# Optimization experiments

Measured on AMD Instinct MI355X. Metric: run time of the kernel, lower is better.

The kernel has to match this reference:

```python
import jax, jax.numpy as jnp
import numpy as np

N_NODES = 100000
N_EDGES = 3200000
IN_C, HID_C, OUT_C = 64, 64, 32


def setup_inputs() -> dict:
    key = jax.random.key(0)
    ks = jax.random.split(key, 8)
    x = jax.random.normal(ks[0], (N_NODES, IN_C), dtype=jnp.float32)
    edge_index = jax.random.randint(ks[1], (2, N_EDGES), 0, N_NODES, dtype=jnp.int64)
    s1 = 1.0 / np.sqrt(IN_C)
    s2 = 1.0 / np.sqrt(HID_C)
    W1l = jax.random.uniform(ks[2], (IN_C, HID_C), jnp.float32, -s1, s1)
    b1l = jnp.zeros((HID_C,), jnp.float32)
    W1r = jax.random.uniform(ks[3], (IN_C, HID_C), jnp.float32, -s1, s1)
    W2l = jax.random.uniform(ks[4], (HID_C, OUT_C), jnp.float32, -s2, s2)
    b2l = jnp.zeros((OUT_C,), jnp.float32)
    W2r = jax.random.uniform(ks[5], (HID_C, OUT_C), jnp.float32, -s2, s2)
    return {"x": x, "edge_index": edge_index, "W1l": W1l, "b1l": b1l,
            "W1r": W1r, "W2l": W2l, "b2l": b2l, "W2r": W2r}


def _sage_conv(x, src, dst, Wl, bl, Wr):
    # mean-aggregate source features onto destination nodes
    msg = x[src]                                              # [E, d] gather
    summed = jax.ops.segment_sum(msg, dst, num_segments=N_NODES)
    deg = jax.ops.segment_sum(jnp.ones((src.shape[0],), x.dtype), dst,
                              num_segments=N_NODES)
    agg = summed / jnp.maximum(deg, 1.0)[:, None]             # [N, d]
    return agg @ Wl + bl + x @ Wr                             # lin_l(agg)+lin_r(x)


def reference(x, edge_index, W1l, b1l, W1r, W2l, b2l, W2r):
    src, dst = edge_index[0], edge_index[1]
    h = jax.nn.relu(_sage_conv(x, src, dst, W1l, b1l, W1r))
    # dropout is identity in eval mode
    return _sage_conv(h, src, dst, W2l, b2l, W2r)
```

## Files before the change

### kernel.cpp

```cpp
#include <hip/hip_runtime.h>
#include <hip/hip_bf16.h>

#define N_NODES 100000
#define N_EDGES 3200000
#define NBKT 391
#define BKT_CAP 10240

typedef __hip_bfloat16 bf16;
typedef unsigned int uint;
typedef __attribute__((ext_vector_type(8))) short bf16x8;
typedef __attribute__((ext_vector_type(4))) float f32x4;

__device__ __forceinline__ float b2f(bf16 v) { return __bfloat162float(v); }

__device__ __forceinline__ float bits2f(unsigned short w) {
    union { unsigned short u; bf16 b; } c;
    c.u = w;
    return __bfloat162float(c.b);
}
__device__ __forceinline__ unsigned short f2bits(float f) {
    return (unsigned short)(__float_as_uint(f) >> 16);
}
__device__ __forceinline__ unsigned short f2bf_bits(float f) {
    bf16 b = __float2bfloat16(f);
    unsigned short u;
    __builtin_memcpy(&u, &b, 2);
    return u;
}

__device__ __forceinline__ int get_idx(const void* ei, long long pos, int is64) {
    if (is64) return (int)((const long long*)ei)[pos];
    return ((const int*)ei)[pos];
}
__device__ __forceinline__ float get_f(const void* p, long long pos, int isbf) {
    if (isbf) return b2f(((const bf16*)p)[pos]);
    return ((const float*)p)[pos];
}

__global__ void detect_kernel(const void* __restrict__ x,
                              const void* __restrict__ ei,
                              int* __restrict__ flags) {
    int lane = threadIdx.x;
    const unsigned short* xw = (const unsigned short*)x;
    float v = bits2f(xw[2 * lane]);
    bool plaus = (v == v) && fabsf(v) > 1e-3f && fabsf(v) < 1e2f;
    unsigned long long m1 = __ballot(plaus);
    const int* iw = (const int*)ei;
    bool z = (iw[2 * lane + 1] == 0);
    unsigned long long m2 = __ballot(z);
    if (lane == 0) {
        flags[0] = (__popcll(m1) >= 32) ? 1 : 0;
        flags[1] = (__popcll(m2) == 64) ? 1 : 0;
    }
}

__global__ __launch_bounds__(256) void scatterA_kernel(
    const void* __restrict__ ei, int* __restrict__ bucket_cursor,
    uint* __restrict__ bucket_data, const int* __restrict__ flags) {
    __shared__ int lhist[NBKT];
    __shared__ int lbase[NBKT];
    int is64 = flags[1];
    int t = threadIdx.x;
    int chunk0 = blockIdx.x * 8192;

    for (int i = t; i < NBKT; i += 256) lhist[i] = 0;
    __syncthreads();
    for (int j = 0; j < 32; j++) {
        int e = chunk0 + j * 256 + t;
        if (e < N_EDGES) {
            int d = get_idx(ei, (long long)N_EDGES + e, is64);
            atomicAdd(&lhist[d >> 8], 1);
        }
    }
    __syncthreads();
    for (int i = t; i < NBKT; i += 256) {
        int c = lhist[i];
        lbase[i] = c ? atomicAdd(&bucket_cursor[i], c) : 0;
        lhist[i] = 0;
    }
    __syncthreads();
    for (int j = 0; j < 32; j++) {
        int e = chunk0 + j * 256 + t;
        if (e < N_EDGES) {
            int s = get_idx(ei, e, is64);
            int d = get_idx(ei, (long long)N_EDGES + e, is64);
            int b = d >> 8;
            int o = lbase[b] + atomicAdd(&lhist[b], 1);
            if (o < BKT_CAP)
                bucket_data[(long long)b * BKT_CAP + o] = ((uint)(d & 255) << 17) | (uint)s;
        }
    }
}

__global__ void scanBuckets_kernel(const int* __restrict__ cnt,
                                   int* __restrict__ base) {
    __shared__ int buf[512];
    int t = threadIdx.x;
    int v = (t < NBKT) ? cnt[t] : 0;
    buf[t] = v;
    __syncthreads();
    for (int off = 1; off < 512; off <<= 1) {
        int add = (t >= off) ? buf[t - off] : 0;
        __syncthreads();
        buf[t] += add;
        __syncthreads();
    }
    if (t < NBKT) base[t] = buf[t] - v;
}

__global__ __launch_bounds__(256) void csrB_kernel(
    const int* __restrict__ bucket_cnt, const int* __restrict__ bucket_base,
    const uint* __restrict__ bucket_data, int* __restrict__ csr_src,
    int* __restrict__ row_start) {
    __shared__ int lh[256];
    __shared__ int buf[256];
    int b = blockIdx.x;
    int t = threadIdx.x;
    int cnt = bucket_cnt[b];
    if (cnt > BKT_CAP) cnt = BKT_CAP;
    int base = bucket_base[b];
    const uint* bd = bucket_data + (long long)b * BKT_CAP;

    lh[t] = 0;
    __syncthreads();
    for (int i = t; i < cnt; i += 256) atomicAdd(&lh[bd[i] >> 17], 1);
    __syncthreads();
    int v = lh[t];
    buf[t] = v;
    __syncthreads();
    for (int off = 1; off < 256; off <<= 1) {
        int add = (t >= off) ? buf[t - off] : 0;
        __syncthreads();
        buf[t] += add;
        __syncthreads();
    }
    int excl = buf[t] - v;
    int g = (b << 8) + t;
    if (g < N_NODES) row_start[g] = base + excl;
    lh[t] = excl;
    __syncthreads();
    for (int i = t; i < cnt; i += 256) {
        uint e = bd[i];
        int o = atomicAdd(&lh[e >> 17], 1);
        csr_src[base + o] = (int)(e & 0x1FFFFu);
    }
    if (b == 0 && t == 0) row_start[N_NODES] = N_EDGES;
}

__global__ __launch_bounds__(256) void node1_kernel(
    const void* __restrict__ x, const int* __restrict__ row_start,
    const int* __restrict__ csr_src, const void* __restrict__ W1l,
    const void* __restrict__ b1l, const void* __restrict__ W1r,
    const void* __restrict__ W2l, const void* __restrict__ b2l,
    const void* __restrict__ W2r, bf16* __restrict__ zbuf,
    bf16* __restrict__ rbuf, const int* __restrict__ flags) {
    __shared__ __align__(16) unsigned short sW1t[64][136];
    __shared__ __align__(16) unsigned short sA[64][136];
    __shared__ __align__(16) unsigned short sW2t[64][72];
    __shared__ __align__(16) unsigned short sH[64][72];
    __shared__ float sB1[64];
    __shared__ float sB2[32];

    int isbf = flags[0];
    int t = threadIdx.x;

    for (int i = t; i < 64 * 128; i += 256) {
        int n = i & 63, k = i >> 6;
        unsigned short v;
        if (isbf)
            v = (k < 64) ? ((const unsigned short*)W1l)[k * 64 + n]
                         : ((const unsigned short*)W1r)[(k - 64) * 64 + n];
        else
            v = f2bits((k < 64) ? ((const float*)W1l)[k * 64 + n]
                                : ((const float*)W1r)[(k - 64) * 64 + n]);
        sW1t[n][k] = v;
    }
    for (int i = t; i < 64 * 64; i += 256) {
        int n = i & 63, k = i >> 6;
        unsigned short v;
        if (isbf)
            v = (n < 32) ? ((const unsigned short*)W2l)[k * 32 + n]
                         : ((const unsigned short*)W2r)[k * 32 + (n - 32)];
        else
            v = f2bits((n < 32) ? ((const float*)W2l)[k * 32 + n]
                                : ((const float*)W2r)[k * 32 + (n - 32)]);
        sW2t[n][k] = v;
    }
    if (t < 64) sB1[t] = get_f(b1l, t, isbf);
    if (t < 32) sB2[t] = get_f(b2l, t, isbf);

    int w = t >> 6, lane = t & 63;
    int mbase = w * 16;
    int n0 = blockIdx.x * 64;
    const uint4* xr4 = (const uint4*)x;
    int e8 = lane >> 3, q8 = lane & 7;
    int e4 = lane >> 4, q16 = lane & 15;

    for (int i = 0; i < 16; i++) {
        int m = mbase + i;
        int n = n0 + m;
        float acc[8] = {0, 0, 0, 0, 0, 0, 0, 0};
        int dg = 0;
        int start = 0, end = 0;
        if (n < N_NODES) {
            start = row_start[n];
            end = row_start[n + 1];
            dg = end - start;
        }
        float av = 0.0f, xv = 0.0f;
        if (isbf) {
            for (int base = start; base < end; base += 32) {
                int i0 = base + e8, i1 = i0 + 8, i2 = i0 + 16, i3 = i0 + 24;
                int s0 = (i0 < end) ? csr_src[i0] : -1;
                int s1 = (i1 < end) ? csr_src[i1] : -1;
                int s2 = (i2 < end) ? csr_src[i2] : -1;
                int s3 = (i3 < end) ? csr_src[i3] : -1;
                uint4 v0 = {0,0,0,0}, v1 = {0,0,0,0}, v2 = {0,0,0,0}, v3 = {0,0,0,0};
                if (s0 >= 0) v0 = xr4[s0 * 8 + q8];
                if (s1 >= 0) v1 = xr4[s1 * 8 + q8];
                if (s2 >= 0) v2 = xr4[s2 * 8 + q8];
                if (s3 >= 0) v3 = xr4[s3 * 8 + q8];
                acc[0] += __uint_as_float(v0.x << 16) + __uint_as_float(v1.x << 16)
                        + __uint_as_float(v2.x << 16) + __uint_as_float(v3.x << 16);
                acc[1] += __uint_as_float(v0.x & 0xffff0000u) + __uint_as_float(v1.x & 0xffff0000u)
                        + __uint_as_float(v2.x & 0xffff0000u) + __uint_as_float(v3.x & 0xffff0000u);
                acc[2] += __uint_as_float(v0.y << 16) + __uint_as_float(v1.y << 16)
                        + __uint_as_float(v2.y << 16) + __uint_as_float(v3.y << 16);
                acc[3] += __uint_as_float(v0.y & 0xffff0000u) + __uint_as_float(v1.y & 0xffff0000u)
                        + __uint_as_float(v2.y & 0xffff0000u) + __uint_as_float(v3.y & 0xffff0000u);
                acc[4] += __uint_as_float(v0.z << 16) + __uint_as_float(v1.z << 16)
                        + __uint_as_float(v2.z << 16) + __uint_as_float(v3.z << 16);
                acc[5] += __uint_as_float(v0.z & 0xffff0000u) + __uint_as_float(v1.z & 0xffff0000u)
                        + __uint_as_float(v2.z & 0xffff0000u) + __uint_as_float(v3.z & 0xffff0000u);
                acc[6] += __uint_as_float(v0.w << 16) + __uint_as_float(v1.w << 16)
                        + __uint_as_float(v2.w << 16) + __uint_as_float(v3.w << 16);
                acc[7] += __uint_as_float(v0.w & 0xffff0000u) + __uint_as_float(v1.w & 0xffff0000u)
                        + __uint_as_float(v2.w & 0xffff0000u) + __uint_as_float(v3.w & 0xffff0000u);
            }
#pragma unroll
            for (int mm = 8; mm <= 32; mm <<= 1)
#pragma unroll
                for (int k = 0; k < 8; k++) acc[k] += __shfl_xor(acc[k], mm, 64);
#pragma unroll
            for (int k = 0; k < 8; k++) {
                float v = __shfl(acc[k], lane >> 3, 64);
                av = ((lane & 7) == k) ? v : av;
            }
            if (n < N_NODES) xv = b2f(((const bf16*)x)[(long long)n * 64 + lane]);
        } else {
            const uint4* xf = (const uint4*)x;
            for (int base = start; base < end; base += 16) {
                int i0 = base + e4, i1 = i0 + 4, i2 = i0 + 8, i3 = i0 + 12;
                int s0 = (i0 < end) ? csr_src[i0] : -1;
                int s1 = (i1 < end) ? csr_src[i1] : -1;
                int s2 = (i2 < end) ? csr_src[i2] : -1;
                int s3 = (i3 < end) ? csr_src[i3] : -1;
                uint4 v0 = {0,0,0,0}, v1 = {0,0,0,0}, v2 = {0,0,0,0}, v3 = {0,0,0,0};
                if (s0 >= 0) v0 = xf[s0 * 16 + q16];
                if (s1 >= 0) v1 = xf[s1 * 16 + q16];
                if (s2 >= 0) v2 = xf[s2 * 16 + q16];
                if (s3 >= 0) v3 = xf[s3 * 16 + q16];
                acc[0] += __uint_as_float(v0.x) + __uint_as_float(v1.x)
                        + __uint_as_float(v2.x) + __uint_as_float(v3.x);
                acc[1] += __uint_as_float(v0.y) + __uint_as_float(v1.y)
                        + __uint_as_float(v2.y) + __uint_as_float(v3.y);
                acc[2] += __uint_as_float(v0.z) + __uint_as_float(v1.z)
                        + __uint_as_float(v2.z) + __uint_as_float(v3.z);
                acc[3] += __uint_as_float(v0.w) + __uint_as_float(v1.w)
                        + __uint_as_float(v2.w) + __uint_as_float(v3.w);
            }
#pragma unroll
            for (int mm = 16; mm <= 32; mm <<= 1)
#pragma unroll
                for (int k = 0; k < 4; k++) acc[k] += __shfl_xor(acc[k], mm, 64);
#pragma unroll
            for (int k = 0; k < 4; k++) {
                float v = __shfl(acc[k], lane >> 2, 64);
                av = ((lane & 3) == k) ? v : av;
            }
            if (n < N_NODES) xv = ((const float*)x)[(long long)n * 64 + lane];
        }
        av *= 1.0f / fmaxf((float)dg, 1.0f);
        sA[m][lane] = f2bf_bits(av);
        sA[m][64 + lane] = f2bf_bits(xv);
    }
    __syncthreads();

    int q = lane >> 4, r15 = lane & 15;
    f32x4 acc1[4] = {{0,0,0,0},{0,0,0,0},{0,0,0,0},{0,0,0,0}};
#pragma unroll
    for (int ks = 0; ks < 4; ks++) {
        bf16x8 afrag = *(const bf16x8*)&sA[mbase + r15][ks * 32 + q * 8];
#pragma unroll
        for (int nt = 0; nt < 4; nt++) {
            bf16x8 bfrag = *(const bf16x8*)&sW1t[nt * 16 + r15][ks * 32 + q * 8];
            acc1[nt] = __builtin_amdgcn_mfma_f32_16x16x32_bf16(afrag, bfrag, acc1[nt], 0, 0, 0);
        }
    }
#pragma unroll
    for (int nt = 0; nt < 4; nt++) {
        int col = nt * 16 + r15;
        float bias = sB1[col];
#pragma unroll
        for (int rr = 0; rr < 4; rr++) {
            int m = mbase + q * 4 + rr;
            sH[m][col] = f2bf_bits(fmaxf(acc1[nt][rr] + bias, 0.0f));
        }
    }
    __syncthreads();

    f32x4 acc2[4] = {{0,0,0,0},{0,0,0,0},{0,0,0,0},{0,0,0,0}};
#pragma unroll
    for (int ks = 0; ks < 2; ks++) {
        bf16x8 afrag = *(const bf16x8*)&sH[mbase + r15][ks * 32 + q * 8];
#pragma unroll
        for (int nt = 0; nt < 4; nt++) {
            bf16x8 bfrag = *(const bf16x8*)&sW2t[nt * 16 + r15][ks * 32 + q * 8];
            acc2[nt] = __builtin_amdgcn_mfma_f32_16x16x32_bf16(afrag, bfrag, acc2[nt], 0, 0, 0);
        }
    }
#pragma unroll
    for (int nt = 0; nt < 4; nt++) {
        int col = nt * 16 + r15;
#pragma unroll
        for (int rr = 0; rr < 4; rr++) {
            int m = mbase + q * 4 + rr;
            int n = n0 + m;
            if (n < N_NODES) {
                float v = acc2[nt][rr];
                if (col < 32)
                    zbuf[(long long)n * 32 + col] = __float2bfloat16(v);
                else
                    rbuf[(long long)n * 32 + (col - 32)] = __float2bfloat16(v + sB2[col - 32]);
            }
        }
    }
}

__global__ void node2_kernel(const int* __restrict__ row_start,
                             const int* __restrict__ csr_src,
                             const bf16* __restrict__ z,
                             const bf16* __restrict__ rbuf,
                             void* __restrict__ out,
                             const int* __restrict__ flags) {
    int isbf = flags[0];
    int t = threadIdx.x;
    int lane = t & 63;
    int e = lane >> 2, q = lane & 3;
    int gw = (blockIdx.x * blockDim.x + t) >> 6;
    int nwaves = (gridDim.x * blockDim.x) >> 6;
    const uint4* zr = (const uint4*)z;

    for (int n = gw; n < N_NODES; n += nwaves) {
        int start = row_start[n];
        int end = row_start[n + 1];
        float acc[8] = {0, 0, 0, 0, 0, 0, 0, 0};
        for (int base = start; base < end; base += 32) {
            int i0 = base + e, i1 = base + 16 + e;
            int s0 = (i0 < end) ? csr_src[i0] : -1;
            int s1 = (i1 < end) ? csr_src[i1] : -1;
            uint4 v0 = {0, 0, 0, 0}, v1 = {0, 0, 0, 0};
            if (s0 >= 0) v0 = zr[s0 * 4 + q];
            if (s1 >= 0) v1 = zr[s1 * 4 + q];
            acc[0] += __uint_as_float(v0.x << 16) + __uint_as_float(v1.x << 16);
            acc[1] += __uint_as_float(v0.x & 0xffff0000u) + __uint_as_float(v1.x & 0xffff0000u);
            acc[2] += __uint_as_float(v0.y << 16) + __uint_as_float(v1.y << 16);
            acc[3] += __uint_as_float(v0.y & 0xffff0000u) + __uint_as_float(v1.y & 0xffff0000u);
            acc[4] += __uint_as_float(v0.z << 16) + __uint_as_float(v1.z << 16);
            acc[5] += __uint_as_float(v0.z & 0xffff0000u) + __uint_as_float(v1.z & 0xffff0000u);
            acc[6] += __uint_as_float(v0.w << 16) + __uint_as_float(v1.w << 16);
            acc[7] += __uint_as_float(v0.w & 0xffff0000u) + __uint_as_float(v1.w & 0xffff0000u);
        }
#pragma unroll
        for (int m = 4; m <= 32; m <<= 1)
#pragma unroll
            for (int k = 0; k < 8; k++) acc[k] += __shfl_xor(acc[k], m, 64);
        float sv = 0.0f;
#pragma unroll
        for (int k = 0; k < 8; k++) {
            float v = __shfl(acc[k], lane >> 3, 64);
            sv = ((lane & 7) == k) ? v : sv;
        }
        if (lane < 32) {
            float invd = 1.0f / fmaxf((float)(end - start), 1.0f);
            float val = sv * invd + b2f(rbuf[n * 32 + lane]);
            if (isbf)
                ((bf16*)out)[n * 32 + lane] = __float2bfloat16(val);
            else
                ((float*)out)[n * 32 + lane] = val;
        }
    }
}

extern "C" void kernel_launch(void* const* d_in, const int* in_sizes, int n_in,
                              void* d_out, int out_size, void* d_ws, size_t ws_size,
                              hipStream_t stream) {
    const void* x = d_in[0];
    const void* ei = d_in[1];
    const void* W1l = d_in[2];
    const void* b1l = d_in[3];
    const void* W1r = d_in[4];
    const void* W2l = d_in[5];
    const void* b2l = d_in[6];
    const void* W2r = d_in[7];

    char* ws = (char*)d_ws;
    uint* bucket_data = (uint*)ws;
    int* csr_src = (int*)(ws + 16015424);
    int* row_start = (int*)(ws + 28815424);
    int* bucket_cursor = (int*)(ws + 29215488);
    int* bucket_base = (int*)(ws + 29217088);
    bf16* zbuf = (bf16*)(ws + 29218688);
    bf16* rbuf = (bf16*)(ws + 35618688);
    int* flags = (int*)(ws + 42018688);

    hipMemsetAsync(bucket_cursor, 0, NBKT * 4, stream);

    detect_kernel<<<1, 64, 0, stream>>>(x, ei, flags);
    scatterA_kernel<<<NBKT, 256, 0, stream>>>(ei, bucket_cursor, bucket_data, flags);
    scanBuckets_kernel<<<1, 512, 0, stream>>>(bucket_cursor, bucket_base);
    csrB_kernel<<<NBKT, 256, 0, stream>>>(bucket_cursor, bucket_base, bucket_data,
                                          csr_src, row_start);
    node1_kernel<<<1563, 256, 0, stream>>>(x, row_start, csr_src, W1l, b1l, W1r,
                                           W2l, b2l, W2r, zbuf, rbuf, flags);
    node2_kernel<<<8192, 256, 0, stream>>>(row_start, csr_src, zbuf, rbuf, d_out,
                                           flags);
}
```

Before: 411.4 us.

## Split layer-1 gather from GEMM into separate kernels with wave-per-node grid

After: 377.0 us. -8.4%, faster.

```diff
diff --git a/kernel.cpp b/kernel.cpp
--- a/kernel.cpp
+++ b/kernel.cpp
@@ -147,67 +147,25 @@
     if (b == 0 && t == 0) row_start[N_NODES] = N_EDGES;
 }
 
-__global__ __launch_bounds__(256) void node1_kernel(
+__global__ __launch_bounds__(256) void gather1_kernel(
     const void* __restrict__ x, const int* __restrict__ row_start,
-    const int* __restrict__ csr_src, const void* __restrict__ W1l,
-    const void* __restrict__ b1l, const void* __restrict__ W1r,
-    const void* __restrict__ W2l, const void* __restrict__ b2l,
-    const void* __restrict__ W2r, bf16* __restrict__ zbuf,
-    bf16* __restrict__ rbuf, const int* __restrict__ flags) {
-    __shared__ __align__(16) unsigned short sW1t[64][136];
-    __shared__ __align__(16) unsigned short sA[64][136];
-    __shared__ __align__(16) unsigned short sW2t[64][72];
-    __shared__ __align__(16) unsigned short sH[64][72];
-    __shared__ float sB1[64];
-    __shared__ float sB2[32];
-
+    const int* __restrict__ csr_src, bf16* __restrict__ aggbuf,
+    const int* __restrict__ flags) {
     int isbf = flags[0];
     int t = threadIdx.x;
-
-    for (int i = t; i < 64 * 128; i += 256) {
-        int n = i & 63, k = i >> 6;
-        unsigned short v;
-        if (isbf)
-            v = (k < 64) ? ((const unsigned short*)W1l)[k * 64 + n]
-                         : ((const unsigned short*)W1r)[(k - 64) * 64 + n];
-        else
-            v = f2bits((k < 64) ? ((const float*)W1l)[k * 64 + n]
-                                : ((const float*)W1r)[(k - 64) * 64 + n]);
-        sW1t[n][k] = v;
-    }
-    for (int i = t; i < 64 * 64; i += 256) {
-        int n = i & 63, k = i >> 6;
-        unsigned short v;
-        if (isbf)
-            v = (n < 32) ? ((const unsigned short*)W2l)[k * 32 + n]
-                         : ((const unsigned short*)W2r)[k * 32 + (n - 32)];
-        else
-            v = f2bits((n < 32) ? ((const float*)W2l)[k * 32 + n]
-                                : ((const float*)W2r)[k * 32 + (n - 32)]);
-        sW2t[n][k] = v;
-    }
-    if (t < 64) sB1[t] = get_f(b1l, t, isbf);
-    if (t < 32) sB2[t] = get_f(b2l, t, isbf);
-
-    int w = t >> 6, lane = t & 63;
-    int mbase = w * 16;
-    int n0 = blockIdx.x * 64;
-    const uint4* xr4 = (const uint4*)x;
+    int lane = t & 63;
+    int gw = (blockIdx.x * 256 + t) >> 6;
+    int nw = (gridDim.x * 256) >> 6;
     int e8 = lane >> 3, q8 = lane & 7;
     int e4 = lane >> 4, q16 = lane & 15;
-
-    for (int i = 0; i < 16; i++) {
-        int m = mbase + i;
-        int n = n0 + m;
+    const uint4* xr4 = (const uint4*)x;
+
+    for (int n = gw; n < N_NODES; n += nw) {
+        int start = row_start[n];
+        int end = row_start[n + 1];
+        int dg = end - start;
         float acc[8] = {0, 0, 0, 0, 0, 0, 0, 0};
-        int dg = 0;
-        int start = 0, end = 0;
-        if (n < N_NODES) {
-            start = row_start[n];
-            end = row_start[n + 1];
-            dg = end - start;
-        }
-        float av = 0.0f, xv = 0.0f;
+        float av = 0.0f;
         if (isbf) {
             for (int base = start; base < end; base += 32) {
                 int i0 = base + e8, i1 = i0 + 8, i2 = i0 + 16, i3 = i0 + 24;
@@ -246,7 +204,6 @@
                 float v = __shfl(acc[k], lane >> 3, 64);
                 av = ((lane & 7) == k) ? v : av;
             }
-            if (n < N_NODES) xv = b2f(((const bf16*)x)[(long long)n * 64 + lane]);
         } else {
             const uint4* xf = (const uint4*)x;
             for (int base = start; base < end; base += 16) {
@@ -278,14 +235,82 @@
                 float v = __shfl(acc[k], lane >> 2, 64);
                 av = ((lane & 3) == k) ? v : av;
             }
-            if (n < N_NODES) xv = ((const float*)x)[(long long)n * 64 + lane];
         }
         av *= 1.0f / fmaxf((float)dg, 1.0f);
-        sA[m][lane] = f2bf_bits(av);
-        sA[m][64 + lane] = f2bf_bits(xv);
-    }
-    __syncthreads();
-
+        aggbuf[(long long)n * 64 + lane] = __float2bfloat16(av);
+    }
+}
+
+__global__ __launch_bounds__(256) void gemm1_kernel(
+    const void* __restrict__ x, const bf16* __restrict__ aggbuf,
+    const void* __restrict__ W1l, const void* __restrict__ b1l,
+    const void* __restrict__ W1r, const void* __restrict__ W2l,
+    const void* __restrict__ b2l, const void* __restrict__ W2r,
+    bf16* __restrict__ zbuf, bf16* __restrict__ rbuf,
+    const int* __restrict__ flags) {
+    __shared__ __align__(16) unsigned short sW1t[64][136];
+    __shared__ __align__(16) unsigned short sA[64][136];
+    __shared__ __align__(16) unsigned short sW2t[64][72];
+    __shared__ __align__(16) unsigned short sH[64][72];
+    __shared__ float sB1[64];
+    __shared__ float sB2[32];
+
+    int isbf = flags[0];
+    int t = threadIdx.x;
+    int n0 = blockIdx.x * 64;
+
+    for (int i = t; i < 64 * 128; i += 256) {
+        int n = i & 63, k = i >> 6;
+        unsigned short v;
+        if (isbf)
+            v = (k < 64) ? ((const unsigned short*)W1l)[k * 64 + n]
+                         : ((const unsigned short*)W1r)[(k - 64) * 64 + n];
+        else
+            v = f2bits((k < 64) ? ((const float*)W1l)[k * 64 + n]
+                                : ((const float*)W1r)[(k - 64) * 64 + n]);
+        sW1t[n][k] = v;
+    }
+    for (int i = t; i < 64 * 64; i += 256) {
+        int n = i & 63, k = i >> 6;
+        unsigned short v;
+        if (isbf)
+            v = (n < 32) ? ((const unsigned short*)W2l)[k * 32 + n]
+                         : ((const unsigned short*)W2r)[k * 32 + (n - 32)];
+        else
+            v = f2bits((n < 32) ? ((const float*)W2l)[k * 32 + n]
+                                : ((const float*)W2r)[k * 32 + (n - 32)]);
+        sW2t[n][k] = v;
+    }
+    if (t < 64) sB1[t] = get_f(b1l, t, isbf);
+    if (t < 32) sB2[t] = get_f(b2l, t, isbf);
+
+    const uint4* ag4 = (const uint4*)aggbuf;
+    if (isbf) {
+        const uint4* x4 = (const uint4*)x;
+        for (int i = t; i < 64 * 16; i += 256) {
+            int m = i >> 4, c = i & 15;
+            int nn = min(n0 + m, N_NODES - 1);
+            uint4 v = (c < 8) ? ag4[(long long)nn * 8 + c]
+                              : x4[(long long)nn * 8 + (c - 8)];
+            *(uint4*)&sA[m][c * 8] = v;
+        }
+    } else {
+        for (int i = t; i < 64 * 8; i += 256) {
+            int m = i >> 3, c = i & 7;
+            int nn = min(n0 + m, N_NODES - 1);
+            *(uint4*)&sA[m][c * 8] = ag4[(long long)nn * 8 + c];
+        }
+        const float* xf = (const float*)x;
+        for (int i = t; i < 64 * 64; i += 256) {
+            int m = i >> 6, c = i & 63;
+            int nn = min(n0 + m, N_NODES - 1);
+            sA[m][64 + c] = f2bf_bits(xf[(long long)nn * 64 + c]);
+        }
+    }
+    __syncthreads();
+
+    int w = t >> 6, lane = t & 63;
+    int mbase = w * 16;
     int q = lane >> 4, r15 = lane & 15;
     f32x4 acc1[4] = {{0,0,0,0},{0,0,0,0},{0,0,0,0},{0,0,0,0}};
 #pragma unroll
@@ -406,6 +431,7 @@
 
     char* ws = (char*)d_ws;
     uint* bucket_data = (uint*)ws;
+    bf16* aggbuf = (bf16*)ws;
     int* csr_src = (int*)(ws + 16015424);
     int* row_start = (int*)(ws + 28815424);
     int* bucket_cursor = (int*)(ws + 29215488);
@@ -421,8 +447,9 @@
     scanBuckets_kernel<<<1, 512, 0, stream>>>(bucket_cursor, bucket_base);
     csrB_kernel<<<NBKT, 256, 0, stream>>>(bucket_cursor, bucket_base, bucket_data,
                                           csr_src, row_start);
-    node1_kernel<<<1563, 256, 0, stream>>>(x, row_start, csr_src, W1l, b1l, W1r,
-                                           W2l, b2l, W2r, zbuf, rbuf, flags);
+    gather1_kernel<<<6250, 256, 0, stream>>>(x, row_start, csr_src, aggbuf, flags);
+    gemm1_kernel<<<1563, 256, 0, stream>>>(x, aggbuf, W1l, b1l, W1r, W2l, b2l,
+                                           W2r, zbuf, rbuf, flags);
     node2_kernel<<<8192, 256, 0, stream>>>(row_start, csr_src, zbuf, rbuf, d_out,
                                            flags);
 }
```
